# Kernel tuning notes

Hardware: AMD Instinct MI355X
Metric: run time of the kernel (lower is better)

Reference implementation:

```python
import jax, jax.numpy as jnp
import numpy as np

N = 100000   # n_nodes
E = 1600000  # n_edges (avg degree 16)
IN, HID, OUT = 128, 128, 64


def setup_inputs() -> dict:
    key = jax.random.key(0)
    k0, k1, k2, k3 = jax.random.split(key, 4)
    x = jax.random.normal(k0, (N, IN), dtype=jnp.float32)
    edge_index = jax.random.randint(k1, (2, E), 0, N, dtype=jnp.int32)
    # Glorot-ish init for GCNConv weights, zero bias (PyG default bias=True)
    W1 = jax.random.normal(k2, (IN, HID), dtype=jnp.float32) * (1.0 / np.sqrt(IN))
    b1 = jnp.zeros((HID,), dtype=jnp.float32)
    W2 = jax.random.normal(k3, (HID, OUT), dtype=jnp.float32) * (1.0 / np.sqrt(HID))
    b2 = jnp.zeros((OUT,), dtype=jnp.float32)
    return {"x": x, "W1": W1, "b1": b1, "W2": W2, "b2": b2, "edge_index": edge_index}


def gcn_layer(x, W, b, src, dst):
    """PyG GCNConv: add self-loops, symmetric deg^{-1/2} normalization,
    linear transform, scatter-add aggregation at dst, plus bias."""
    n = x.shape[0]
    h = x @ W                                   # [n, d_out]
    loops = jnp.arange(n, dtype=src.dtype)
    s = jnp.concatenate([src, loops])           # sources incl. self-loops
    d = jnp.concatenate([dst, loops])           # targets incl. self-loops
    deg = jax.ops.segment_sum(jnp.ones_like(d, dtype=h.dtype), d, num_segments=n)
    dinv = jnp.where(deg > 0, jax.lax.rsqrt(deg), 0.0)
    norm = dinv[s] * dinv[d]                    # [E+n]
    msg = h[s] * norm[:, None]                  # gather + scale
    out = jax.ops.segment_sum(msg, d, num_segments=n)  # scatter-add
    return out + b


def reference(x, W1, b1, W2, b2, edge_index):
    src, dst = edge_index[0], edge_index[1]
    h = jax.nn.relu(gcn_layer(x, W1, b1, src, dst))
    return gcn_layer(h, W2, b2, src, dst)
```

## Files before the change

kernel.cpp:

```cpp
#include <hip/hip_runtime.h>

#define NNODES 100000
#define NEDGES 1600000
#define IND 128
#define HIDD 128
#define OUTD 64

#define BSHIFT 8
#define BSIZE  256
#define NBUCK  ((NNODES + BSIZE - 1) / BSIZE)
#define SLACK  4800
#define SEG_CAP 5120
#define BIN_EPB 8192
#define BINB   ((NEDGES + BIN_EPB - 1) / BIN_EPB)
#define GEMMB  ((NNODES + 127) / 128)
#define WT2B   ((HIDD * OUTD + 511) / 512)

typedef unsigned int  uint32;
typedef __attribute__((ext_vector_type(8))) short short8;
typedef __attribute__((ext_vector_type(4))) float floatx4;
typedef __attribute__((ext_vector_type(4))) unsigned int uivec4;
typedef __attribute__((ext_vector_type(4))) float fvec4;

__device__ __forceinline__ unsigned short f2bf(float f) {
    union { float f; uint32 u; } x; x.f = f;
    uint32 u = x.u;
    return (unsigned short)((u + 0x7fffu + ((u >> 16) & 1u)) >> 16);
}
__device__ __forceinline__ float bflo(uint32 u) {
    union { uint32 i; float f; } x; x.i = u << 16; return x.f;
}
__device__ __forceinline__ float bfhi(uint32 u) {
    union { uint32 i; float f; } x; x.i = u & 0xffff0000u; return x.f;
}

__launch_bounds__(512)
__global__ void k_bin_gemm(const int* __restrict__ src, const int* __restrict__ dst,
                           int* __restrict__ bcnt, uint32* __restrict__ staging, int e,
                           const float* __restrict__ x, const float* __restrict__ W1,
                           const float* __restrict__ W2, unsigned short* __restrict__ wt2,
                           unsigned short* __restrict__ C, int n) {
    constexpr int K = IND;
    constexpr int KP = K + 8;
    constexpr int M = HIDD;
    constexpr int NT = M / 16;
    __shared__ __align__(16) char smem[2 * 128 * KP * 2];

    const int tid = threadIdx.x;
    const int bid = blockIdx.x;

    if (bid < BINB) {
        int* lh   = (int*)smem;
        int* lcur = lh + NBUCK;
        for (int i = tid; i < NBUCK; i += 512) lh[i] = 0;
        __syncthreads();

        const int start = bid * BIN_EPB;
        const int4* d4 = (const int4*)dst;
        const int4* s4 = (const int4*)src;

        int4 dv[4], sv[4];
        bool val[4];
#pragma unroll
        for (int k = 0; k < 4; k++) {
            int off = start + 4 * (k * 512 + tid);
            val[k] = off < e;
            if (val[k]) { dv[k] = d4[off >> 2]; sv[k] = s4[off >> 2]; }
        }

#pragma unroll
        for (int k = 0; k < 4; k++) {
            if (val[k]) {
                atomicAdd(&lh[dv[k].x >> BSHIFT], 1);
                atomicAdd(&lh[dv[k].y >> BSHIFT], 1);
                atomicAdd(&lh[dv[k].z >> BSHIFT], 1);
                atomicAdd(&lh[dv[k].w >> BSHIFT], 1);
            }
        }
        __syncthreads();

        for (int i = tid; i < NBUCK; i += 512)
            lcur[i] = lh[i] ? atomicAdd(&bcnt[i], lh[i]) : 0;
        __syncthreads();

#pragma unroll
        for (int k = 0; k < 4; k++) {
            if (val[k]) {
                int d, s, b, pos;
                d = dv[k].x; s = sv[k].x; b = d >> BSHIFT;
                pos = atomicAdd(&lcur[b], 1);
                if (pos < SLACK) staging[(size_t)b * SLACK + pos] = ((uint32)(d & (BSIZE - 1)) << 17) | (uint32)s;
                d = dv[k].y; s = sv[k].y; b = d >> BSHIFT;
                pos = atomicAdd(&lcur[b], 1);
                if (pos < SLACK) staging[(size_t)b * SLACK + pos] = ((uint32)(d & (BSIZE - 1)) << 17) | (uint32)s;
                d = dv[k].z; s = sv[k].z; b = d >> BSHIFT;
                pos = atomicAdd(&lcur[b], 1);
                if (pos < SLACK) staging[(size_t)b * SLACK + pos] = ((uint32)(d & (BSIZE - 1)) << 17) | (uint32)s;
                d = dv[k].w; s = sv[k].w; b = d >> BSHIFT;
                pos = atomicAdd(&lcur[b], 1);
                if (pos < SLACK) staging[(size_t)b * SLACK + pos] = ((uint32)(d & (BSIZE - 1)) << 17) | (uint32)s;
            }
        }
        return;
    }

    if (bid >= BINB + GEMMB) {
        int idx = (bid - BINB - GEMMB) * 512 + tid;
        if (idx < HIDD * OUTD) {
            int k = idx / OUTD, m = idx - k * OUTD;
            wt2[m * HIDD + k] = f2bf(W2[idx]);
        }
        return;
    }

    unsigned short* Asl = (unsigned short*)smem;
    unsigned short* Wsl = Asl + 128 * KP;

    const int row0 = (bid - BINB) * 128;

    for (int idx = tid; idx < 128 * 128; idx += 512) {
        int k = idx >> 7, m = idx & 127;
        Wsl[m * KP + k] = f2bf(W1[idx]);
    }
    {
        constexpr int F4R = K / 4;
        for (int idx = tid; idx < 128 * F4R; idx += 512) {
            int r = idx / F4R, s = idx - r * F4R;
            int grow = row0 + r; if (grow >= n) grow = n - 1;
            float4 v = *(const float4*)(x + (size_t)grow * K + s * 4);
            uint32 p0 = (uint32)f2bf(v.x) | ((uint32)f2bf(v.y) << 16);
            uint32 p1 = (uint32)f2bf(v.z) | ((uint32)f2bf(v.w) << 16);
            *(uint2*)(Asl + r * KP + s * 4) = make_uint2(p0, p1);
        }
    }
    __syncthreads();

    const int lane = tid & 63;
    const int wave = tid >> 6;
    const int mm = lane & 15;
    const int qq = lane >> 4;

    floatx4 acc[NT];
#pragma unroll
    for (int t = 0; t < NT; t++) acc[t] = (floatx4){0.f, 0.f, 0.f, 0.f};

#pragma unroll
    for (int kc = 0; kc < K / 32; kc++) {
        short8 a = *(const short8*)(Asl + (wave * 16 + mm) * KP + kc * 32 + qq * 8);
#pragma unroll
        for (int t = 0; t < NT; t++) {
            short8 b = *(const short8*)(Wsl + (t * 16 + mm) * KP + kc * 32 + qq * 8);
            acc[t] = __builtin_amdgcn_mfma_f32_16x16x32_bf16(a, b, acc[t], 0, 0, 0);
        }
    }

#pragma unroll
    for (int r = 0; r < 4; r++) {
        int grow = row0 + wave * 16 + qq * 4 + r;
        if (grow < n) {
#pragma unroll
            for (int t = 0; t < NT; t++)
                C[(size_t)grow * M + t * 16 + mm] = f2bf(acc[t][r]);
        }
    }
}

__global__ __launch_bounds__(256)
void k_fill3(const uint32* __restrict__ staging, const int* __restrict__ bcnt,
             int* __restrict__ row_ptr, int* __restrict__ csr_src,
             float* __restrict__ dinv, int n) {
    __shared__ int nc[BSIZE];
    __shared__ int lcur[BSIZE];
    __shared__ int red[256];
    __shared__ int wsum[4];
    __shared__ int seg[SEG_CAP];
    const int b = blockIdx.x;
    const int base = b << BSHIFT;
    const int tid = threadIdx.x;

    nc[tid] = 0;

    int t0 = (tid < b) ? bcnt[tid] : 0;
    int t1 = (tid + 256 < b) ? bcnt[tid + 256] : 0;
    red[tid] = t0 + t1;
    __syncthreads();
    for (int off = 128; off > 0; off >>= 1) {
        if (tid < off) red[tid] += red[tid + off];
        __syncthreads();
    }
    const int r0 = red[0];

    const uint32* st = staging + (size_t)b * SLACK;
    const int cnt = bcnt[b];
    for (int i = tid; i < cnt; i += 256)
        atomicAdd(&nc[st[i] >> 17], 1);
    __syncthreads();

    const int lane = tid & 63;
    const int w = tid >> 6;
    int dg = nc[tid];
    int v = dg;
#pragma unroll
    for (int off = 1; off < 64; off <<= 1) {
        int t = __shfl_up(v, off);
        if (lane >= off) v += t;
    }
    if (lane == 63) wsum[w] = v;
    __syncthreads();
    if (tid == 0) {
        int a = 0;
#pragma unroll
        for (int i = 0; i < 4; i++) { int t = wsum[i]; wsum[i] = a; a += t; }
    }
    __syncthreads();
    const int inc = v + wsum[w];
    const int ex = inc - dg;
    const int vnode = base + tid;
    if (vnode < n) {
        row_ptr[vnode] = r0 + ex;
        dinv[vnode] = rsqrtf((float)(dg + 1));
    }
    lcur[tid] = ex;
    if (b == NBUCK - 1 && tid == 255) row_ptr[n] = r0 + inc;
    __syncthreads();

    for (int i = tid; i < cnt; i += 256) {
        uint32 p = st[i];
        int dl = (int)(p >> 17);
        int s  = (int)(p & 0x1FFFFu);
        int pos = atomicAdd(&lcur[dl], 1);
        if (pos < SEG_CAP) seg[pos] = s;
        else               csr_src[r0 + pos] = s;
    }
    __syncthreads();
    int lim = min(cnt, SEG_CAP);
    for (int i = tid; i < lim; i += 256) csr_src[r0 + i] = seg[i];
}

__launch_bounds__(256)
__global__ void gather_gemm(const unsigned short* __restrict__ h,
                            const int* __restrict__ row_ptr,
                            const int* __restrict__ csr_src,
                            const float* __restrict__ dinv,
                            const float* __restrict__ bias1,
                            const unsigned short* __restrict__ WT2,
                            unsigned short* __restrict__ C2, int n) {
    constexpr int K  = HIDD;
    constexpr int KP = K + 8;
    constexpr int M2 = OUTD;
    __shared__ unsigned short Atl[16 * KP];
    __shared__ unsigned short Wsl[M2 * KP];

    const int tid = threadIdx.x;

    {
        constexpr int SEG = (K * 2) / 16;
        const uint4* srcp = (const uint4*)WT2;
        for (int idx = tid; idx < M2 * SEG; idx += 256) {
            int r = idx / SEG, s = idx - r * SEG;
            *(uint4*)(Wsl + r * KP + s * 8) = srcp[idx];
        }
    }

    const int g = tid >> 4;
    const int l = tid & 15;
    const int v0 = blockIdx.x * 16;
    const int v = v0 + g;

    uint4 pk = make_uint4(0u, 0u, 0u, 0u);
    if (v < n) {
        const float dv = dinv[v];
        float acc[8];
        {
            uint4 u = *(const uint4*)(h + (size_t)v * K + l * 8);
            acc[0] = dv * bflo(u.x); acc[1] = dv * bfhi(u.x);
            acc[2] = dv * bflo(u.y); acc[3] = dv * bfhi(u.y);
            acc[4] = dv * bflo(u.z); acc[5] = dv * bfhi(u.z);
            acc[6] = dv * bflo(u.w); acc[7] = dv * bfhi(u.w);
        }

        int j   = row_ptr[v];
        int end = row_ptr[v + 1];
        for (; j + 3 < end; j += 4) {
            int s0 = csr_src[j];
            int s1 = csr_src[j + 1];
            int s2 = csr_src[j + 2];
            int s3 = csr_src[j + 3];
            float q0 = dinv[s0], q1 = dinv[s1], q2 = dinv[s2], q3 = dinv[s3];
            uint4 u0 = *(const uint4*)(h + (size_t)s0 * K + l * 8);
            uint4 u1 = *(const uint4*)(h + (size_t)s1 * K + l * 8);
            uint4 u2 = *(const uint4*)(h + (size_t)s2 * K + l * 8);
            uint4 u3 = *(const uint4*)(h + (size_t)s3 * K + l * 8);
            acc[0] += (q0 * bflo(u0.x) + q1 * bflo(u1.x)) + (q2 * bflo(u2.x) + q3 * bflo(u3.x));
            acc[1] += (q0 * bfhi(u0.x) + q1 * bfhi(u1.x)) + (q2 * bfhi(u2.x) + q3 * bfhi(u3.x));
            acc[2] += (q0 * bflo(u0.y) + q1 * bflo(u1.y)) + (q2 * bflo(u2.y) + q3 * bflo(u3.y));
            acc[3] += (q0 * bfhi(u0.y) + q1 * bfhi(u1.y)) + (q2 * bfhi(u2.y) + q3 * bfhi(u3.y));
            acc[4] += (q0 * bflo(u0.z) + q1 * bflo(u1.z)) + (q2 * bflo(u2.z) + q3 * bflo(u3.z));
            acc[5] += (q0 * bfhi(u0.z) + q1 * bfhi(u1.z)) + (q2 * bfhi(u2.z) + q3 * bfhi(u3.z));
            acc[6] += (q0 * bflo(u0.w) + q1 * bflo(u1.w)) + (q2 * bflo(u2.w) + q3 * bflo(u3.w));
            acc[7] += (q0 * bfhi(u0.w) + q1 * bfhi(u1.w)) + (q2 * bfhi(u2.w) + q3 * bfhi(u3.w));
        }
        for (; j < end; j++) {
            int s0 = csr_src[j];
            float q0 = dinv[s0];
            uint4 u0 = *(const uint4*)(h + (size_t)s0 * K + l * 8);
            acc[0] += q0 * bflo(u0.x); acc[1] += q0 * bfhi(u0.x);
            acc[2] += q0 * bflo(u0.y); acc[3] += q0 * bfhi(u0.y);
            acc[4] += q0 * bflo(u0.z); acc[5] += q0 * bfhi(u0.z);
            acc[6] += q0 * bflo(u0.w); acc[7] += q0 * bfhi(u0.w);
        }

#pragma unroll
        for (int i = 0; i < 8; i++) {
            acc[i] = fmaxf(acc[i] * dv + bias1[l * 8 + i], 0.0f);
        }
        pk.x = (uint32)f2bf(acc[0]) | ((uint32)f2bf(acc[1]) << 16);
        pk.y = (uint32)f2bf(acc[2]) | ((uint32)f2bf(acc[3]) << 16);
        pk.z = (uint32)f2bf(acc[4]) | ((uint32)f2bf(acc[5]) << 16);
        pk.w = (uint32)f2bf(acc[6]) | ((uint32)f2bf(acc[7]) << 16);
    }
    *(uint4*)(Atl + g * KP + l * 8) = pk;
    __syncthreads();

    const int lane = tid & 63;
    const int wv = tid >> 6;
    const int mm = lane & 15;
    const int qq = lane >> 4;

    floatx4 o = (floatx4){0.f, 0.f, 0.f, 0.f};
#pragma unroll
    for (int kc = 0; kc < K / 32; kc++) {
        short8 a = *(const short8*)(Atl + mm * KP + kc * 32 + qq * 8);
        short8 b = *(const short8*)(Wsl + (wv * 16 + mm) * KP + kc * 32 + qq * 8);
        o = __builtin_amdgcn_mfma_f32_16x16x32_bf16(a, b, o, 0, 0, 0);
    }

#pragma unroll
    for (int r = 0; r < 4; r++) {
        int grow = v0 + qq * 4 + r;
        if (grow < n) {
            float dv2 = dinv[grow];
            C2[(size_t)grow * M2 + wv * 16 + mm] = f2bf(o[r] * dv2);
        }
    }
}

template<int M, bool RELU, bool OBF16>
__launch_bounds__(256)
__global__ void gather_k(const unsigned short* __restrict__ h,
                         const int* __restrict__ row_ptr,
                         const int* __restrict__ csr_src,
                         const float* __restrict__ dinv,
                         const float* __restrict__ bias,
                         void* __restrict__ outp, int n) {
    constexpr int LPG = M / 8;
    constexpr int GPB = 256 / LPG;
    const int g = threadIdx.x / LPG;
    const int l = threadIdx.x % LPG;
    const int v = blockIdx.x * GPB + g;
    if (v >= n) return;

    const float dv = dinv[v];
    float acc[8];
    {
        uint4 u = *(const uint4*)(h + (size_t)v * M + l * 8);
        acc[0] = bflo(u.x); acc[1] = bfhi(u.x);
        acc[2] = bflo(u.y); acc[3] = bfhi(u.y);
        acc[4] = bflo(u.z); acc[5] = bfhi(u.z);
        acc[6] = bflo(u.w); acc[7] = bfhi(u.w);
    }

    int j   = row_ptr[v];
    int end = row_ptr[v + 1];
    for (; j + 3 < end; j += 4) {
        int s0 = csr_src[j];
        int s1 = csr_src[j + 1];
        int s2 = csr_src[j + 2];
        int s3 = csr_src[j + 3];
        uint4 u0 = *(const uint4*)(h + (size_t)s0 * M + l * 8);
        uint4 u1 = *(const uint4*)(h + (size_t)s1 * M + l * 8);
        uint4 u2 = *(const uint4*)(h + (size_t)s2 * M + l * 8);
        uint4 u3 = *(const uint4*)(h + (size_t)s3 * M + l * 8);
        acc[0] += (bflo(u0.x) + bflo(u1.x)) + (bflo(u2.x) + bflo(u3.x));
        acc[1] += (bfhi(u0.x) + bfhi(u1.x)) + (bfhi(u2.x) + bfhi(u3.x));
        acc[2] += (bflo(u0.y) + bflo(u1.y)) + (bflo(u2.y) + bflo(u3.y));
        acc[3] += (bfhi(u0.y) + bfhi(u1.y)) + (bfhi(u2.y) + bfhi(u3.y));
        acc[4] += (bflo(u0.z) + bflo(u1.z)) + (bflo(u2.z) + bflo(u3.z));
        acc[5] += (bfhi(u0.z) + bfhi(u1.z)) + (bfhi(u2.z) + bfhi(u3.z));
        acc[6] += (bflo(u0.w) + bflo(u1.w)) + (bflo(u2.w) + bflo(u3.w));
        acc[7] += (bfhi(u0.w) + bfhi(u1.w)) + (bfhi(u2.w) + bfhi(u3.w));
    }
    for (; j < end; j++) {
        int s0 = csr_src[j];
        uint4 u0 = *(const uint4*)(h + (size_t)s0 * M + l * 8);
        acc[0] += bflo(u0.x); acc[1] += bfhi(u0.x);
        acc[2] += bflo(u0.y); acc[3] += bfhi(u0.y);
        acc[4] += bflo(u0.z); acc[5] += bfhi(u0.z);
        acc[6] += bflo(u0.w); acc[7] += bfhi(u0.w);
    }

#pragma unroll
    for (int i = 0; i < 8; i++) {
        acc[i] = acc[i] * dv + bias[l * 8 + i];
        if (RELU) acc[i] = fmaxf(acc[i], 0.0f);
    }

    if constexpr (OBF16) {
        uivec4 p;
#pragma unroll
        for (int c = 0; c < 4; c++)
            p[c] = (uint32)f2bf(acc[2 * c]) | ((uint32)f2bf(acc[2 * c + 1]) << 16);
        __builtin_nontemporal_store(p,
            (uivec4*)((unsigned short*)outp + (size_t)v * M + l * 8));
    } else {
        float* op = (float*)outp + (size_t)v * M + l * 8;
        fvec4 a0 = {acc[0], acc[1], acc[2], acc[3]};
        fvec4 a1 = {acc[4], acc[5], acc[6], acc[7]};
        __builtin_nontemporal_store(a0, (fvec4*)op);
        __builtin_nontemporal_store(a1, (fvec4*)(op + 4));
    }
}

extern "C" void kernel_launch(void* const* d_in, const int* in_sizes, int n_in,
                              void* d_out, int out_size, void* d_ws, size_t ws_size,
                              hipStream_t stream) {
    const float* x  = (const float*)d_in[0];
    const float* W1 = (const float*)d_in[1];
    const float* b1 = (const float*)d_in[2];
    const float* W2 = (const float*)d_in[3];
    const float* b2 = (const float*)d_in[4];
    const int*   ei = (const int*)d_in[5];
    const int* src = ei;
    const int* dst = ei + NEDGES;
    float* out = (float*)d_out;

    char* ws = (char*)d_ws;
    float*  dinv    = (float*)ws;   ws += (size_t)NNODES * 4;
    int*    row_ptr = (int*)ws;     ws += (size_t)(NNODES + 4) * 4;
    int*    bcnt    = (int*)ws;     ws += 512 * 4;
    unsigned short* wt2 = (unsigned short*)ws;  ws += (size_t)HIDD * OUTD * 2;
    int*    csr_src = (int*)ws;     ws += (size_t)NEDGES * 4;
    uint32* staging = (uint32*)ws;  ws += (size_t)NBUCK * SLACK * 4;
    unsigned short* hbf1 = (unsigned short*)ws; ws += (size_t)NNODES * HIDD * 2;
    unsigned short* hbf2 = (unsigned short*)ws;

    hipMemsetAsync(bcnt, 0, 512 * 4, stream);
    k_bin_gemm<<<BINB + GEMMB + WT2B, 512, 0, stream>>>(
        src, dst, bcnt, staging, NEDGES, x, W1, W2, wt2, hbf1, NNODES);

    k_fill3<<<NBUCK, 256, 0, stream>>>(staging, bcnt, row_ptr, csr_src, dinv, NNODES);

    gather_gemm<<<(NNODES + 15) / 16, 256, 0, stream>>>(
        hbf1, row_ptr, csr_src, dinv, b1, wt2, hbf2, NNODES);

    gather_k<OUTD, false, false><<<(NNODES * (OUTD / 8) + 255) / 256, 256, 0, stream>>>(
        hbf2, row_ptr, csr_src, dinv, b2, out, NNODES);
}
```

Baseline: 279.6 us.

## Locally sort binned edges in LDS before coalesced writes to staging

The binning blocks now run a block-wide prefix scan over their per-bucket counts and place each edge into a bucket-sorted array in shared memory. A second pass then copies the entries to global staging, so consecutive threads write consecutive addresses within each bucket's reserved range. The goal is to replace scattered 4-byte global stores with mostly contiguous runs. The cost is a 9-step scan with barriers, about 48KB more LDS use (which must fit the shared buffer), and an extra LDS pass.

After: 275.4 us, median of 2. About the same (-1.5%).

```diff
diff --git a/kernel.cpp b/kernel.cpp
--- a/kernel.cpp
+++ b/kernel.cpp
@@ -50,12 +50,19 @@
     const int bid = blockIdx.x;
 
     if (bid < BINB) {
-        int* lh   = (int*)smem;
-        int* lcur = lh + NBUCK;
+        int* lh     = (int*)smem;
+        int* lstart = lh + NBUCK;
+        int* lcur   = lstart + NBUCK;
+        int* gres   = lcur + NBUCK;
+        int* sbuf   = gres + NBUCK;
+        uint32* ent = (uint32*)(sbuf + 512);
+        unsigned short* bkt = (unsigned short*)(ent + BIN_EPB);
+
         for (int i = tid; i < NBUCK; i += 512) lh[i] = 0;
         __syncthreads();
 
         const int start = bid * BIN_EPB;
+        const int end = min(start + BIN_EPB, e);
         const int4* d4 = (const int4*)dst;
         const int4* s4 = (const int4*)src;
 
@@ -79,8 +86,21 @@
         }
         __syncthreads();
 
-        for (int i = tid; i < NBUCK; i += 512)
-            lcur[i] = lh[i] ? atomicAdd(&bcnt[i], lh[i]) : 0;
+        int vb = (tid < NBUCK) ? lh[tid] : 0;
+        sbuf[tid] = vb;
+        __syncthreads();
+        for (int off = 1; off < 512; off <<= 1) {
+            int t = (tid >= off) ? sbuf[tid - off] : 0;
+            __syncthreads();
+            sbuf[tid] += t;
+            __syncthreads();
+        }
+        if (tid < NBUCK) {
+            int ex = sbuf[tid] - vb;
+            lstart[tid] = ex;
+            lcur[tid]   = ex;
+            gres[tid]   = vb ? atomicAdd(&bcnt[tid], vb) : 0;
+        }
         __syncthreads();
 
 #pragma unroll
@@ -89,17 +109,30 @@
                 int d, s, b, pos;
                 d = dv[k].x; s = sv[k].x; b = d >> BSHIFT;
                 pos = atomicAdd(&lcur[b], 1);
-                if (pos < SLACK) staging[(size_t)b * SLACK + pos] = ((uint32)(d & (BSIZE - 1)) << 17) | (uint32)s;
+                ent[pos] = ((uint32)(d & (BSIZE - 1)) << 17) | (uint32)s;
+                bkt[pos] = (unsigned short)b;
                 d = dv[k].y; s = sv[k].y; b = d >> BSHIFT;
                 pos = atomicAdd(&lcur[b], 1);
-                if (pos < SLACK) staging[(size_t)b * SLACK + pos] = ((uint32)(d & (BSIZE - 1)) << 17) | (uint32)s;
+                ent[pos] = ((uint32)(d & (BSIZE - 1)) << 17) | (uint32)s;
+                bkt[pos] = (unsigned short)b;
                 d = dv[k].z; s = sv[k].z; b = d >> BSHIFT;
                 pos = atomicAdd(&lcur[b], 1);
-                if (pos < SLACK) staging[(size_t)b * SLACK + pos] = ((uint32)(d & (BSIZE - 1)) << 17) | (uint32)s;
+                ent[pos] = ((uint32)(d & (BSIZE - 1)) << 17) | (uint32)s;
+                bkt[pos] = (unsigned short)b;
                 d = dv[k].w; s = sv[k].w; b = d >> BSHIFT;
                 pos = atomicAdd(&lcur[b], 1);
-                if (pos < SLACK) staging[(size_t)b * SLACK + pos] = ((uint32)(d & (BSIZE - 1)) << 17) | (uint32)s;
+                ent[pos] = ((uint32)(d & (BSIZE - 1)) << 17) | (uint32)s;
+                bkt[pos] = (unsigned short)b;
             }
+        }
+        __syncthreads();
+
+        const int total = end - start;
+        for (int i = tid; i < total; i += 512) {
+            int b = bkt[i];
+            int p = gres[b] + (i - lstart[b]);
+            if (p < SLACK)
+                staging[(size_t)b * SLACK + p] = ent[i];
         }
         return;
     }
```
